# Kernel optimization log

Hardware: AMD Instinct MI355X
Metric: run time of the kernel (lower is better)

The kernel has to match this reference:

```python
import jax, jax.numpy as jnp
import numpy as np

NORM_EPS = 1e-6
QUANT_EPS = 1e-8


def setup_inputs() -> dict:
    key = jax.random.key(0)
    k1, k2 = jax.random.split(key)
    B, S, D_IN, D_OUT = 2, 4096, 2048, 2048
    x = jax.random.normal(k1, (B, S, D_IN), dtype=jnp.float32)
    # master fp32 weights (kaiming-uniform-ish scale)
    weight = jax.random.uniform(k2, (D_OUT, D_IN), dtype=jnp.float32,
                                minval=-1.0, maxval=1.0) * (1.0 / np.sqrt(D_IN))
    norm_weight = jnp.ones((D_IN,), dtype=jnp.float32)
    return {"x": x, "weight": weight, "norm_weight": norm_weight}


def _rmsnorm(x, gain):
    rms = jnp.sqrt(jnp.mean(x * x, axis=-1, keepdims=True) + NORM_EPS)
    return x / rms * gain


def _ternary_quantize(w):
    gamma = jnp.mean(jnp.abs(w))                       # absmean scale (scalar)
    w_q = jnp.clip(jnp.round(w / (gamma + QUANT_EPS)), -1.0, 1.0)
    return w_q, gamma


def reference(x, weight, norm_weight):
    # 1) RMSNorm input
    xn = _rmsnorm(x, norm_weight)
    # 2) ternary-quantize weights {-1,0,+1} with absmean gamma
    w_q, gamma = _ternary_quantize(weight)
    # 3) matmul with ternary weights, 4) scale by gamma
    # xn: [B,S,Din], w_q: [Dout,Din] -> [B,S,Dout]
    return jnp.einsum('bsd,od->bso', xn, w_q) * gamma
```

## Files before the change

kernel.cpp:

```cpp
#include <hip/hip_runtime.h>
#include <hip/hip_bf16.h>
#include <stdint.h>

typedef unsigned short u16;
typedef signed char i8;

#define D_INNER 2048
#define D_OUTER 2048
#define MROWS   8192
#define W_ELEMS (D_OUTER * D_INNER)
#define NPART   1024

#define BM 256
#define BN 256
#define BK 64
#define NKT (D_INNER / BK)
#define SLOT_BYTES 32768
#define LDS_TOTAL  131072

typedef __attribute__((ext_vector_type(4))) float f32x4;
typedef __attribute__((ext_vector_type(4))) int   i32x4;
typedef __attribute__((ext_vector_type(16))) int  i32x16;

__global__ __launch_bounds__(256) void prep_kernel(const float* __restrict__ x,
                            const float* __restrict__ g,
                            const float* __restrict__ w,
                            i8* __restrict__ xn, float* __restrict__ srow,
                            float* __restrict__ partials) {
  __shared__ float red[4];
  __shared__ float redm[4];
  int t = threadIdx.x;
  int lane = t & 63, wvi = t >> 6;

  if (blockIdx.x >= MROWS) {
    int p = blockIdx.x - MROWS;
    int base = p * 1024;
    float s = 0.f;
#pragma unroll
    for (int r = 0; r < 4; ++r) {
      f32x4 v = ((const f32x4*)w)[base + r * 256 + t];
      s += fabsf(v[0]) + fabsf(v[1]) + fabsf(v[2]) + fabsf(v[3]);
    }
    for (int off = 32; off; off >>= 1) s += __shfl_down(s, off, 64);
    if (lane == 0) red[wvi] = s;
    __syncthreads();
    if (t == 0) partials[p] = red[0] + red[1] + red[2] + red[3];
    return;
  }

  int row = blockIdx.x;
  const f32x4* xr = (const f32x4*)(x + (size_t)row * D_INNER);
  i8* xo = xn + (size_t)row * D_INNER;

  f32x4 v0 = __builtin_nontemporal_load(&xr[t]);
  f32x4 v1 = __builtin_nontemporal_load(&xr[t + 256]);
  const f32x4* gr = (const f32x4*)g;
  f32x4 g0 = gr[t], g1 = gr[t + 256];

  float s = v0[0]*v0[0] + v0[1]*v0[1] + v0[2]*v0[2] + v0[3]*v0[3]
          + v1[0]*v1[0] + v1[1]*v1[1] + v1[2]*v1[2] + v1[3]*v1[3];
  float m = fmaxf(fmaxf(fmaxf(fabsf(v0[0]*g0[0]), fabsf(v0[1]*g0[1])),
                        fmaxf(fabsf(v0[2]*g0[2]), fabsf(v0[3]*g0[3]))),
                  fmaxf(fmaxf(fabsf(v1[0]*g1[0]), fabsf(v1[1]*g1[1])),
                        fmaxf(fabsf(v1[2]*g1[2]), fabsf(v1[3]*g1[3]))));
  for (int off = 32; off; off >>= 1) {
    s += __shfl_down(s, off, 64);
    m = fmaxf(m, __shfl_down(m, off, 64));
  }
  if (lane == 0) { red[wvi] = s; redm[wvi] = m; }
  __syncthreads();
  float total = red[0] + red[1] + red[2] + red[3];
  float rmax  = fmaxf(fmaxf(redm[0], redm[1]), fmaxf(redm[2], redm[3]));
  float invr = 1.0f / sqrtf(total * (1.0f / (float)D_INNER) + 1e-6f);

  float amax = fmaxf(rmax * invr, 1e-12f);
  float step = amax * (1.0f / 127.0f);
  float qs   = 127.0f / amax;
  if (t == 0) srow[row] = step;

  char4 q0, q1;
  float qv;
  qv = fminf(127.f, fmaxf(-127.f, rintf(v0[0]*invr*g0[0]*qs))); q0.x = (i8)(int)qv;
  qv = fminf(127.f, fmaxf(-127.f, rintf(v0[1]*invr*g0[1]*qs))); q0.y = (i8)(int)qv;
  qv = fminf(127.f, fmaxf(-127.f, rintf(v0[2]*invr*g0[2]*qs))); q0.z = (i8)(int)qv;
  qv = fminf(127.f, fmaxf(-127.f, rintf(v0[3]*invr*g0[3]*qs))); q0.w = (i8)(int)qv;
  qv = fminf(127.f, fmaxf(-127.f, rintf(v1[0]*invr*g1[0]*qs))); q1.x = (i8)(int)qv;
  qv = fminf(127.f, fmaxf(-127.f, rintf(v1[1]*invr*g1[1]*qs))); q1.y = (i8)(int)qv;
  qv = fminf(127.f, fmaxf(-127.f, rintf(v1[2]*invr*g1[2]*qs))); q1.z = (i8)(int)qv;
  qv = fminf(127.f, fmaxf(-127.f, rintf(v1[3]*invr*g1[3]*qs))); q1.w = (i8)(int)qv;
  ((char4*)xo)[t]       = q0;
  ((char4*)xo)[t + 256] = q1;
}

__global__ __launch_bounds__(256) void quant_kernel(const float* __restrict__ w,
                             const float* __restrict__ partials,
                             float* __restrict__ gamma_out, i8* __restrict__ wq) {
  f32x4 pv = ((const f32x4*)partials)[threadIdx.x];
  double d = (double)pv[0] + (double)pv[1] + (double)pv[2] + (double)pv[3];
  for (int off = 32; off; off >>= 1) d += __shfl_down(d, off, 64);
  __shared__ double red[4];
  int lane = threadIdx.x & 63, wvi = threadIdx.x >> 6;
  if (lane == 0) red[wvi] = d;
  __syncthreads();
  double total = red[0] + red[1] + red[2] + red[3];
  float gamma = (float)(total * (1.0 / (double)W_ELEMS));
  float inv = 1.0f / (gamma + 1e-8f);
  if (blockIdx.x == 0 && threadIdx.x == 0) *gamma_out = gamma;

  int tid = blockIdx.x * blockDim.x + threadIdx.x;
  int stride = gridDim.x * blockDim.x;
  for (int i = tid; i < W_ELEMS / 4; i += stride) {
    f32x4 v = ((const f32x4*)w)[i];
    char4 q;
    q.x = (i8)(int)fminf(1.f, fmaxf(-1.f, rintf(v[0] * inv)));
    q.y = (i8)(int)fminf(1.f, fmaxf(-1.f, rintf(v[1] * inv)));
    q.z = (i8)(int)fminf(1.f, fmaxf(-1.f, rintf(v[2] * inv)));
    q.w = (i8)(int)fminf(1.f, fmaxf(-1.f, rintf(v[3] * inv)));
    ((char4*)wq)[i] = q;
  }
}

#define GLDS(SRC, DST) __builtin_amdgcn_global_load_lds( \
    (const __attribute__((address_space(1))) void*)(SRC), \
    (__attribute__((address_space(3))) void*)(DST), 16, 0, 0)
#define WAITVM(N) asm volatile("s_waitcnt vmcnt(" #N ")")
#define BAR()     __builtin_amdgcn_s_barrier()
#define FENCE()   __builtin_amdgcn_sched_barrier(0)

__global__ __launch_bounds__(512, 2) void gemm_bt(const i8* __restrict__ A,
                                                  const i8* __restrict__ Bw,
                                                  const float* __restrict__ gamma_p,
                                                  const float* __restrict__ srow,
                                                  float* __restrict__ C) {
  extern __shared__ i8 lds[];

  int f   = blockIdx.y * 8 + blockIdx.x;
  int xcd = f & 7;
  int g   = f >> 3;
  int orig = xcd * 32 + g;
  int nb  = orig & 7;
  int mb  = orig >> 3;
  int bm0 = mb * BM;
  int bn0 = nb * BN;

  int tid  = threadIdx.x;
  int lane = tid & 63;
  int wv   = tid >> 6;
  int wr   = wv >> 2;
  int wc   = wv & 3;
  int l31  = lane & 31;
  int hi   = lane >> 5;
  int wr4  = wr * 4;
  int wc2  = wc * 2;

  const i8* Ag = A  + (size_t)bm0 * D_INNER;
  const i8* Bg = Bw + (size_t)bn0 * D_INNER;

  int srow_ = ((tid >> 6) & 7) * 32 + (tid & 31);
  int sg_   = (tid >> 5) & 1;
  size_t off0 = (size_t)srow_ * D_INNER + sg_ * 16;
  int dst0 = tid * 16;

  int rdoff = (hi * 32 + l31) * 16;

  i32x16 acc[4][2] = {};

#define STAGE(T_, S_) do { \
    const i8* ap_ = Ag + (size_t)(T_) * BK + off0; \
    const i8* bp_ = Bg + (size_t)(T_) * BK + off0; \
    i8* sa_ = lds + (S_) * SLOT_BYTES + dst0; \
    GLDS(ap_,      sa_);          \
    GLDS(ap_ + 32, sa_ + 8192);   \
    GLDS(bp_,      sa_ + 16384);  \
    GLDS(bp_ + 32, sa_ + 24576);  \
  } while (0)

#define TILE_COMPUTE(T_) do { \
    const i8* sl_ = lds + ((T_) & 3) * SLOT_BYTES; \
    i32x4 af[2][4], bf[2][2]; \
    _Pragma("unroll") for (int ks = 0; ks < 2; ++ks) { \
      _Pragma("unroll") for (int mi = 0; mi < 4; ++mi) \
        af[ks][mi] = *(const i32x4*)(sl_ + ks * 8192 + (wr4 + mi) * 1024 + rdoff); \
      _Pragma("unroll") for (int nj = 0; nj < 2; ++nj) \
        bf[ks][nj] = *(const i32x4*)(sl_ + 16384 + ks * 8192 + (wc2 + nj) * 1024 + rdoff); \
    } \
    __builtin_amdgcn_s_setprio(1); \
    _Pragma("unroll") for (int ks = 0; ks < 2; ++ks) \
      _Pragma("unroll") for (int mi = 0; mi < 4; ++mi) \
        _Pragma("unroll") for (int nj = 0; nj < 2; ++nj) \
          acc[mi][nj] = __builtin_amdgcn_mfma_i32_32x32x32_i8(af[ks][mi], bf[ks][nj], acc[mi][nj], 0, 0, 0); \
    __builtin_amdgcn_s_setprio(0); \
  } while (0)

  STAGE(0, 0); STAGE(1, 1); STAGE(2, 2);

  for (int t = 0; t < NKT - 3; ++t) {
    STAGE(t + 3, (t + 3) & 3);
    WAITVM(12);
    BAR();
    FENCE();
    TILE_COMPUTE(t);
    FENCE();
    BAR();
  }
  WAITVM(8); BAR(); FENCE(); TILE_COMPUTE(NKT - 3); FENCE(); BAR();
  WAITVM(4); BAR(); FENCE(); TILE_COMPUTE(NKT - 2); FENCE(); BAR();
  WAITVM(0); BAR(); FENCE(); TILE_COMPUTE(NKT - 1);

  float gamma = *gamma_p;
  int colb = bn0 + wc * 64 + l31;
#pragma unroll
  for (int mi = 0; mi < 4; ++mi) {
    int rbase = bm0 + wr * 128 + mi * 32 + hi * 4;
    f32x4 sg[4];
#pragma unroll
    for (int q = 0; q < 4; ++q) {
      f32x4 sv = *(const f32x4*)(srow + rbase + q * 8);
      sg[q] = sv * gamma;
    }
#pragma unroll
    for (int nj = 0; nj < 2; ++nj) {
      i32x16 v = acc[mi][nj];
      float* cp = C + (size_t)rbase * D_OUTER + (colb + nj * 32);
#pragma unroll
      for (int q = 0; q < 4; ++q)
#pragma unroll
        for (int rr = 0; rr < 4; ++rr)
          cp[(size_t)(q * 8 + rr) * D_OUTER] = (float)v[q * 4 + rr] * sg[q][rr];
    }
  }
}

extern "C" void kernel_launch(void* const* d_in, const int* in_sizes, int n_in,
                              void* d_out, int out_size, void* d_ws, size_t ws_size,
                              hipStream_t stream) {
  const float* x = (const float*)d_in[0];
  const float* w = (const float*)d_in[1];
  const float* g = (const float*)d_in[2];
  float* out = (float*)d_out;

  float* gamma_p  = (float*)d_ws;
  float* partials = (float*)((char*)d_ws + 64);
  float* srow     = (float*)((char*)d_ws + 8192);
  i8* xn = (i8*)((char*)d_ws + 8192 + 32768);
  i8* wq = (i8*)((char*)d_ws + 8192 + 32768 + (size_t)MROWS * D_INNER);

  static bool attr_set = false;
  if (!attr_set) {
    (void)hipFuncSetAttribute(reinterpret_cast<const void*>(&gemm_bt),
                              hipFuncAttributeMaxDynamicSharedMemorySize, LDS_TOTAL);
    attr_set = true;
  }

  prep_kernel<<<MROWS + NPART, 256, 0, stream>>>(x, g, w, xn, srow, partials);
  quant_kernel<<<2048, 256, 0, stream>>>(w, partials, gamma_p, wq);
  gemm_bt<<<dim3(8, 32), 512, LDS_TOTAL, stream>>>(xn, wq, gamma_p, srow, out);
}
```

Before: 173.3 us.

## Restructure int8 GEMM main loop with BK=128, swizzled LDS and phased staging

Doubles the K tile to 128 and uses two 64KB LDS slots. Global-to-LDS loads are split into quarter-chunks issued between MFMA phases, and an XOR swizzle on 16-byte chunks is meant to avoid LDS bank conflicts. B fragments are loaded once per tile and reused across four A sub-phases. The aim is fewer barriers per K step and better overlap of loads with MFMA, at the cost of more barriers per phase, complex index arithmetic and a risk of subtle staging-order bugs.

```diff
diff --git a/kernel.cpp b/kernel.cpp
--- a/kernel.cpp
+++ b/kernel.cpp
@@ -13,9 +13,9 @@
 
 #define BM 256
 #define BN 256
-#define BK 64
+#define BK 128
 #define NKT (D_INNER / BK)
-#define SLOT_BYTES 32768
+#define SLOT_BYTES 65536
 #define LDS_TOTAL  131072
 
 typedef __attribute__((ext_vector_type(4))) float f32x4;
@@ -126,6 +126,7 @@
 #define WAITVM(N) asm volatile("s_waitcnt vmcnt(" #N ")")
 #define BAR()     __builtin_amdgcn_s_barrier()
 #define FENCE()   __builtin_amdgcn_sched_barrier(0)
+#define LGKM0()   do { asm volatile("s_waitcnt lgkmcnt(0)"); FENCE(); } while (0)
 
 __global__ __launch_bounds__(512, 2) void gemm_bt(const i8* __restrict__ A,
                                                   const i8* __restrict__ Bw,
@@ -136,8 +137,8 @@
 
   int f   = blockIdx.y * 8 + blockIdx.x;
   int xcd = f & 7;
-  int g   = f >> 3;
-  int orig = xcd * 32 + g;
+  int gg  = f >> 3;
+  int orig = xcd * 32 + gg;
   int nb  = orig & 7;
   int mb  = orig >> 3;
   int bm0 = mb * BM;
@@ -150,62 +151,96 @@
   int wc   = wv & 3;
   int l31  = lane & 31;
   int hi   = lane >> 5;
-  int wr4  = wr * 4;
-  int wc2  = wc * 2;
 
   const i8* Ag = A  + (size_t)bm0 * D_INNER;
   const i8* Bg = Bw + (size_t)bn0 * D_INNER;
 
-  int srow_ = ((tid >> 6) & 7) * 32 + (tid & 31);
-  int sg_   = (tid >> 5) & 1;
-  size_t off0 = (size_t)srow_ * D_INNER + sg_ * 16;
-  int dst0 = tid * 16;
-
-  int rdoff = (hi * 32 + l31) * 16;
+  int s_arow = (tid >> 8) * 128 + ((tid & 255) >> 3);
+  int s_adst = (tid >> 8) * 16384 + (tid & 255) * 16;
+  int s_brow = tid >> 3;
+  int s_chunk = tid & 7;
+
+  int rbyteA = (wr * 128 + l31) * 128;
+  int rbyteB[2];
+  rbyteB[0] = (wc * 64 + l31) * 128;
+  rbyteB[1] = (wc * 64 + 32 + l31) * 128;
+  int swz[4];
+#pragma unroll
+  for (int ks = 0; ks < 4; ++ks)
+    swz[ks] = (((ks << 1) | hi) ^ (l31 & 7)) << 4;
 
   i32x16 acc[4][2] = {};
-
-#define STAGE(T_, S_) do { \
-    const i8* ap_ = Ag + (size_t)(T_) * BK + off0; \
-    const i8* bp_ = Bg + (size_t)(T_) * BK + off0; \
-    i8* sa_ = lds + (S_) * SLOT_BYTES + dst0; \
-    GLDS(ap_,      sa_);          \
-    GLDS(ap_ + 32, sa_ + 8192);   \
-    GLDS(bp_,      sa_ + 16384);  \
-    GLDS(bp_ + 32, sa_ + 24576);  \
-  } while (0)
-
-#define TILE_COMPUTE(T_) do { \
-    const i8* sl_ = lds + ((T_) & 3) * SLOT_BYTES; \
-    i32x4 af[2][4], bf[2][2]; \
-    _Pragma("unroll") for (int ks = 0; ks < 2; ++ks) { \
-      _Pragma("unroll") for (int mi = 0; mi < 4; ++mi) \
-        af[ks][mi] = *(const i32x4*)(sl_ + ks * 8192 + (wr4 + mi) * 1024 + rdoff); \
+  i32x4 bfr[4][2];
+
+#define STAGE_AB(T_, P_, S_) do { \
+    int ar_ = (P_) * 32 + s_arow; \
+    GLDS(Ag + (size_t)ar_ * D_INNER + (T_) * BK + ((s_chunk ^ (ar_ & 7)) << 4), \
+         lds + (S_) * SLOT_BYTES + (P_) * 4096 + s_adst); \
+    int br_ = (P_) * 64 + s_brow; \
+    GLDS(Bg + (size_t)br_ * D_INNER + (T_) * BK + ((s_chunk ^ (br_ & 7)) << 4), \
+         lds + (S_) * SLOT_BYTES + 32768 + (P_) * 8192 + tid * 16); \
+  } while (0)
+
+#define MFMA8(TPH) do { \
+    __builtin_amdgcn_s_setprio(1); \
+    _Pragma("unroll") for (int ks = 0; ks < 4; ++ks) \
       _Pragma("unroll") for (int nj = 0; nj < 2; ++nj) \
-        bf[ks][nj] = *(const i32x4*)(sl_ + 16384 + ks * 8192 + (wc2 + nj) * 1024 + rdoff); \
-    } \
-    __builtin_amdgcn_s_setprio(1); \
-    _Pragma("unroll") for (int ks = 0; ks < 2; ++ks) \
-      _Pragma("unroll") for (int mi = 0; mi < 4; ++mi) \
-        _Pragma("unroll") for (int nj = 0; nj < 2; ++nj) \
-          acc[mi][nj] = __builtin_amdgcn_mfma_i32_32x32x32_i8(af[ks][mi], bf[ks][nj], acc[mi][nj], 0, 0, 0); \
+        acc[(TPH)][nj] = __builtin_amdgcn_mfma_i32_32x32x32_i8( \
+            af_[ks], bfr[ks][nj], acc[(TPH)][nj], 0, 0, 0); \
     __builtin_amdgcn_s_setprio(0); \
   } while (0)
 
-  STAGE(0, 0); STAGE(1, 1); STAGE(2, 2);
-
-  for (int t = 0; t < NKT - 3; ++t) {
-    STAGE(t + 3, (t + 3) & 3);
-    WAITVM(12);
-    BAR();
-    FENCE();
-    TILE_COMPUTE(t);
-    FENCE();
-    BAR();
-  }
-  WAITVM(8); BAR(); FENCE(); TILE_COMPUTE(NKT - 3); FENCE(); BAR();
-  WAITVM(4); BAR(); FENCE(); TILE_COMPUTE(NKT - 2); FENCE(); BAR();
-  WAITVM(0); BAR(); FENCE(); TILE_COMPUTE(NKT - 1);
+#define PHASE0(IT, PP, WAITSTMT, DS_) do { \
+    if (DS_) { int T_ = ((PP) == 0) ? (2 * (IT) + 1) : (2 * (IT) + 2 + ((((PP)-1) & 7) >> 2)); \
+               STAGE_AB(T_, (((PP)-1) & 3), ((((PP)-1) & 7) >> 2)); } \
+    WAITSTMT; \
+    BAR(); \
+    const i8* sb_ = lds + ((PP) >> 2) * SLOT_BYTES; \
+    i32x4 af_[4]; \
+    _Pragma("unroll") for (int ks = 0; ks < 4; ++ks) \
+      af_[ks] = *(const i32x4*)(sb_ + rbyteA + swz[ks]); \
+    _Pragma("unroll") for (int ks = 0; ks < 4; ++ks) \
+      _Pragma("unroll") for (int nj = 0; nj < 2; ++nj) \
+        bfr[ks][nj] = *(const i32x4*)(sb_ + 32768 + rbyteB[nj] + swz[ks]); \
+    LGKM0(); \
+    MFMA8(0); \
+    BAR(); \
+  } while (0)
+
+#define PHASEK(IT, PP, DS_) do { \
+    const i8* sb_ = lds + ((PP) >> 2) * SLOT_BYTES; \
+    i32x4 af_[4]; \
+    _Pragma("unroll") for (int ks = 0; ks < 4; ++ks) \
+      af_[ks] = *(const i32x4*)(sb_ + rbyteA + ((PP) & 3) * 4096 + swz[ks]); \
+    if (DS_) { int T_ = 2 * (IT) + 2 + ((((PP)-1) & 7) >> 2); \
+               STAGE_AB(T_, (((PP)-1) & 3), ((((PP)-1) & 7) >> 2)); } \
+    BAR(); \
+    LGKM0(); \
+    MFMA8((PP) & 3); \
+    BAR(); \
+  } while (0)
+
+  STAGE_AB(0, 0, 0); STAGE_AB(0, 1, 0); STAGE_AB(0, 2, 0); STAGE_AB(0, 3, 0);
+  STAGE_AB(1, 0, 1); STAGE_AB(1, 1, 1); STAGE_AB(1, 2, 1);
+
+  for (int it = 0; it < 7; ++it) {
+    PHASE0(it, 0, WAITVM(8), 1);
+    PHASEK(it, 1, 1);
+    PHASEK(it, 2, 1);
+    PHASEK(it, 3, 1);
+    PHASE0(it, 4, WAITVM(8), 1);
+    PHASEK(it, 5, 1);
+    PHASEK(it, 6, 1);
+    PHASEK(it, 7, 1);
+  }
+  PHASE0(7, 0, WAITVM(8), 1);
+  PHASEK(7, 1, 0);
+  PHASEK(7, 2, 0);
+  PHASEK(7, 3, 0);
+  PHASE0(7, 4, WAITVM(0), 0);
+  PHASEK(7, 5, 0);
+  PHASEK(7, 6, 0);
+  PHASEK(7, 7, 0);
 
   float gamma = *gamma_p;
   int colb = bn0 + wc * 64 + l31;
```

After: 162.7 us. -6.1%, faster.

## Load B fragments directly to registers and double-buffer swizzled A in LDS

Applied to the files above, without the earlier changes.

The int8 GEMM main loop is restructured. The K tile grows to 128 and only A goes through LDS, double-buffered with an XOR swizzle to avoid bank conflicts. B fragments are loaded straight from global memory into registers with inline global_load_dwordx4, ping-ponging between two register sets. The block-to-XCD mapping also changes to group neighbouring tiles. This cuts LDS traffic and footprint, which may allow higher occupancy, but it adds register pressure and relies on hand-tuned vmcnt waits.

```diff
diff --git a/kernel.cpp b/kernel.cpp
--- a/kernel.cpp
+++ b/kernel.cpp
@@ -13,10 +13,9 @@
 
 #define BM 256
 #define BN 256
-#define BK 64
+#define BK 128
 #define NKT (D_INNER / BK)
-#define SLOT_BYTES 32768
-#define LDS_TOTAL  131072
+#define LDS_TOTAL 65536
 
 typedef __attribute__((ext_vector_type(4))) float f32x4;
 typedef __attribute__((ext_vector_type(4))) int   i32x4;
@@ -126,6 +125,10 @@
 #define WAITVM(N) asm volatile("s_waitcnt vmcnt(" #N ")")
 #define BAR()     __builtin_amdgcn_s_barrier()
 #define FENCE()   __builtin_amdgcn_sched_barrier(0)
+#define LGKM0()   do { asm volatile("s_waitcnt lgkmcnt(0)"); FENCE(); } while (0)
+#define BLOAD(DST, PTR, OFFS) \
+  asm volatile("global_load_dwordx4 %0, %1, off offset:" OFFS \
+               : "=v"(DST) : "v"(PTR))
 
 __global__ __launch_bounds__(512, 2) void gemm_bt(const i8* __restrict__ A,
                                                   const i8* __restrict__ Bw,
@@ -136,10 +139,9 @@
 
   int f   = blockIdx.y * 8 + blockIdx.x;
   int xcd = f & 7;
-  int g   = f >> 3;
-  int orig = xcd * 32 + g;
-  int nb  = orig & 7;
-  int mb  = orig >> 3;
+  int gg  = f >> 3;
+  int nb  = (xcd & 1) * 4 + (gg & 3);
+  int mb  = (xcd >> 1) * 8 + (gg >> 2);
   int bm0 = mb * BM;
   int bn0 = nb * BN;
 
@@ -150,62 +152,75 @@
   int wc   = wv & 3;
   int l31  = lane & 31;
   int hi   = lane >> 5;
-  int wr4  = wr * 4;
-  int wc2  = wc * 2;
 
   const i8* Ag = A  + (size_t)bm0 * D_INNER;
   const i8* Bg = Bw + (size_t)bn0 * D_INNER;
 
-  int srow_ = ((tid >> 6) & 7) * 32 + (tid & 31);
-  int sg_   = (tid >> 5) & 1;
-  size_t off0 = (size_t)srow_ * D_INNER + sg_ * 16;
-  int dst0 = tid * 16;
-
-  int rdoff = (hi * 32 + l31) * 16;
+  size_t a_src0 = (size_t)(tid >> 3) * D_INNER + (((tid & 7) ^ ((tid >> 3) & 7)) << 4);
+
+  const i8* pB0 = Bg + (size_t)(wc * 64 +      l31) * D_INNER + hi * 16;
+  const i8* pB1 = Bg + (size_t)(wc * 64 + 32 + l31) * D_INNER + hi * 16;
+
+  int rdA = (wr * 128 + l31) * BK;
+  int swz[4];
+#pragma unroll
+  for (int ks = 0; ks < 4; ++ks)
+    swz[ks] = (((ks << 1) | hi) ^ (l31 & 7)) << 4;
 
   i32x16 acc[4][2] = {};
-
-#define STAGE(T_, S_) do { \
-    const i8* ap_ = Ag + (size_t)(T_) * BK + off0; \
-    const i8* bp_ = Bg + (size_t)(T_) * BK + off0; \
-    i8* sa_ = lds + (S_) * SLOT_BYTES + dst0; \
-    GLDS(ap_,      sa_);          \
-    GLDS(ap_ + 32, sa_ + 8192);   \
-    GLDS(bp_,      sa_ + 16384);  \
-    GLDS(bp_ + 32, sa_ + 24576);  \
-  } while (0)
-
-#define TILE_COMPUTE(T_) do { \
-    const i8* sl_ = lds + ((T_) & 3) * SLOT_BYTES; \
-    i32x4 af[2][4], bf[2][2]; \
-    _Pragma("unroll") for (int ks = 0; ks < 2; ++ks) { \
-      _Pragma("unroll") for (int mi = 0; mi < 4; ++mi) \
-        af[ks][mi] = *(const i32x4*)(sl_ + ks * 8192 + (wr4 + mi) * 1024 + rdoff); \
-      _Pragma("unroll") for (int nj = 0; nj < 2; ++nj) \
-        bf[ks][nj] = *(const i32x4*)(sl_ + 16384 + ks * 8192 + (wc2 + nj) * 1024 + rdoff); \
+  i32x4 bfrA[4][2], bfrB[4][2];
+
+#define STAGE_A(T_, S_) do { \
+    _Pragma("unroll") for (int r = 0; r < 4; ++r) \
+      GLDS(Ag + a_src0 + (size_t)r * (64 * D_INNER) + (size_t)(T_) * BK, \
+           lds + (S_) * 32768 + r * 8192 + tid * 16); \
+  } while (0)
+
+#define BLOAD8(NXT) do { \
+    BLOAD(NXT[0][0], pB0, "0");  BLOAD(NXT[0][1], pB1, "0");  \
+    BLOAD(NXT[1][0], pB0, "32"); BLOAD(NXT[1][1], pB1, "32"); \
+    BLOAD(NXT[2][0], pB0, "64"); BLOAD(NXT[2][1], pB1, "64"); \
+    BLOAD(NXT[3][0], pB0, "96"); BLOAD(NXT[3][1], pB1, "96"); \
+  } while (0)
+
+#define MFMA8(PH, CUR) do { \
+    __builtin_amdgcn_s_setprio(1); \
+    _Pragma("unroll") for (int ks = 0; ks < 4; ++ks) { \
+      acc[PH][0] = __builtin_amdgcn_mfma_i32_32x32x32_i8(af_[ks], CUR[ks][0], acc[PH][0], 0, 0, 0); \
+      acc[PH][1] = __builtin_amdgcn_mfma_i32_32x32x32_i8(af_[ks], CUR[ks][1], acc[PH][1], 0, 0, 0); \
     } \
-    __builtin_amdgcn_s_setprio(1); \
-    _Pragma("unroll") for (int ks = 0; ks < 2; ++ks) \
-      _Pragma("unroll") for (int mi = 0; mi < 4; ++mi) \
-        _Pragma("unroll") for (int nj = 0; nj < 2; ++nj) \
-          acc[mi][nj] = __builtin_amdgcn_mfma_i32_32x32x32_i8(af[ks][mi], bf[ks][nj], acc[mi][nj], 0, 0, 0); \
     __builtin_amdgcn_s_setprio(0); \
   } while (0)
 
-  STAGE(0, 0); STAGE(1, 1); STAGE(2, 2);
-
-  for (int t = 0; t < NKT - 3; ++t) {
-    STAGE(t + 3, (t + 3) & 3);
-    WAITVM(12);
-    BAR();
-    FENCE();
-    TILE_COMPUTE(t);
-    FENCE();
-    BAR();
-  }
-  WAITVM(8); BAR(); FENCE(); TILE_COMPUTE(NKT - 3); FENCE(); BAR();
-  WAITVM(4); BAR(); FENCE(); TILE_COMPUTE(NKT - 2); FENCE(); BAR();
-  WAITVM(0); BAR(); FENCE(); TILE_COMPUTE(NKT - 1);
+#define TILE(T_, CUR, NXT, DO_STAGE, WAITSTMT) do { \
+    if (DO_STAGE) { \
+      BLOAD8(NXT); \
+      STAGE_A((T_) + 1, ((T_) + 1) & 1); \
+      pB0 += BK; pB1 += BK; \
+    } \
+    WAITSTMT; FENCE(); \
+    BAR(); FENCE(); \
+    { const i8* sl_ = lds + ((T_) & 1) * 32768; \
+      _Pragma("unroll") for (int ph = 0; ph < 4; ++ph) { \
+        i32x4 af_[4]; \
+        _Pragma("unroll") for (int ks = 0; ks < 4; ++ks) \
+          af_[ks] = *(const i32x4*)(sl_ + rdA + ph * 4096 + swz[ks]); \
+        LGKM0(); \
+        MFMA8(ph, CUR); \
+      } } \
+    BAR(); \
+  } while (0)
+
+  BLOAD8(bfrA);
+  STAGE_A(0, 0);
+  pB0 += BK; pB1 += BK;
+
+  for (int t = 0; t < 14; t += 2) {
+    TILE(t,     bfrA, bfrB, 1, WAITVM(12));
+    TILE(t + 1, bfrB, bfrA, 1, WAITVM(12));
+  }
+  TILE(14, bfrA, bfrB, 1, WAITVM(12));
+  TILE(15, bfrB, bfrA, 0, WAITVM(0));
 
   float gamma = *gamma_p;
   int colb = bn0 + wc * 64 + l31;
```

New measurement: 178.5 us. 3.0% more time.
